# Kernel tuning notes

Hardware: AMD Instinct MI355X
Metric: run time of the kernel (lower is better)

The kernel has to match this reference:

```python
import jax, jax.numpy as jnp
import numpy as np

N = 50000       # nodes
E = 800000      # edges (before self-loops)
F_IN = 128      # num_features
HID = 32        # hidden_dim per head
HEADS = 8
C = 40          # num_classes
NEG_SLOPE = 0.2 # PyG GATConv default leaky_relu slope


def setup_inputs() -> dict:
    key = jax.random.key(0)
    ks = jax.random.split(key, 10)
    x = jax.random.normal(ks[0], (N, F_IN), jnp.float32)
    edge_index = jax.random.randint(ks[1], (2, E), 0, N, dtype=jnp.int64)
    W1 = jax.random.normal(ks[2], (F_IN, HEADS * HID), jnp.float32) * np.float32(1.0 / np.sqrt(F_IN))
    a1_src = jax.random.normal(ks[3], (HEADS, HID), jnp.float32) * 0.1
    a1_dst = jax.random.normal(ks[4], (HEADS, HID), jnp.float32) * 0.1
    b1 = jnp.zeros((HEADS * HID,), jnp.float32)
    W2 = jax.random.normal(ks[5], (HEADS * HID, C), jnp.float32) * np.float32(1.0 / np.sqrt(HEADS * HID))
    a2_src = jax.random.normal(ks[6], (1, C), jnp.float32) * 0.1
    a2_dst = jax.random.normal(ks[7], (1, C), jnp.float32) * 0.1
    b2 = jnp.zeros((C,), jnp.float32)
    return {"x": x, "edge_index": edge_index,
            "W1": W1, "a1_src": a1_src, "a1_dst": a1_dst, "b1": b1,
            "W2": W2, "a2_src": a2_src, "a2_dst": a2_dst, "b2": b2}


def gat_conv(x, edge_index, W, a_src, a_dst, bias):
    """PyG-style GATConv (concat heads, add_self_loops=True), inference mode (no dropout)."""
    n = x.shape[0]
    heads, out_dim = a_src.shape
    ar = jnp.arange(n, dtype=edge_index.dtype)
    src = jnp.concatenate([edge_index[0], ar])   # [E+N]
    dst = jnp.concatenate([edge_index[1], ar])   # [E+N]
    h = (x @ W).reshape(n, heads, out_dim)       # [N, H, D]
    alpha_src = jnp.einsum('nhd,hd->nh', h, a_src)  # [N, H]
    alpha_dst = jnp.einsum('nhd,hd->nh', h, a_dst)  # [N, H]
    e = jax.nn.leaky_relu(alpha_src[src] + alpha_dst[dst], NEG_SLOPE)  # [E+N, H]
    # segment softmax over edges grouped by destination node
    m = jax.ops.segment_max(e, dst, num_segments=n)          # [N, H]
    ex = jnp.exp(e - m[dst])                                  # [E+N, H]
    s = jax.ops.segment_sum(ex, dst, num_segments=n)          # [N, H]
    alpha = ex / (s[dst] + 1e-16)                              # [E+N, H]
    msg = h[src] * alpha[..., None]                            # [E+N, H, D]
    out = jax.ops.segment_sum(msg, dst, num_segments=n)       # [N, H, D]
    return out.reshape(n, heads * out_dim) + bias


def reference(x, edge_index, W1, a1_src, a1_dst, b1, W2, a2_src, a2_dst, b2):
    h = jax.nn.elu(gat_conv(x, edge_index, W1, a1_src, a1_dst, b1))
    # F.dropout is identity in eval mode
    return gat_conv(h, edge_index, W2, a2_src, a2_dst, b2)
```

## Files before the change

### kernel.cpp

```cpp
#include <hip/hip_runtime.h>
#include <math.h>

#define F_IN 128
#define HID 32
#define HEADS 8
#define HD 256
#define NC 40
#define NCP 48
#define H2S 64
#define CAP 96
#define NEG 0.2f

typedef _Float16 half8 __attribute__((ext_vector_type(8)));
typedef float f32x4 __attribute__((ext_vector_type(4)));

__device__ __forceinline__ float leaky(float v) { return v > 0.0f ? v : NEG * v; }
__device__ __forceinline__ float2 up2(unsigned int u) {
    union { unsigned int u; _Float16 h[2]; } c; c.u = u;
    return make_float2((float)c.h[0], (float)c.h[1]);
}

__global__ __launch_bounds__(256) void prep_scatter_k(const int* __restrict__ ei,
        int* __restrict__ cnt, int* __restrict__ esrc,
        const float* __restrict__ W1, const float* __restrict__ W2,
        const float* __restrict__ a1s, const float* __restrict__ a1d,
        _Float16* __restrict__ W1t, _Float16* __restrict__ W2t,
        _Float16* __restrict__ Pt, int E) {
    int i = blockIdx.x * 256 + threadIdx.x;
    if (i < E) {
        int src = ei[i], dst = ei[E + i];
        int pos = atomicAdd(&cnt[dst], 1);
        esrc[dst * CAP + pos] = src;
        return;
    }
    int w1i = i - E;
    if (w1i < HD * F_IN) {
        int c = w1i >> 7, k = w1i & 127;
        W1t[w1i] = (_Float16)W1[k * HD + c];
        return;
    }
    int w2i = w1i - HD * F_IN;
    if (w2i < NCP * HD) {
        int c = w2i >> 8, k = w2i & 255;
        W2t[w2i] = (c < NC) ? (_Float16)W2[k * NC + c] : (_Float16)0.0f;
        return;
    }
    int p = w2i - NCP * HD;
    if (p < 16 * F_IN) {
        int pj = p >> 7, k = p & 127;
        int h = pj & 7;
        const float* av = (pj < 8) ? (a1s + h * HID) : (a1d + h * HID);
        const float* wr = W1 + (size_t)k * HD + h * HID;
        float acc = 0.0f;
#pragma unroll 8
        for (int d = 0; d < HID; ++d) acc = fmaf(wr[d], av[d], acc);
        Pt[pj * F_IN + k] = (_Float16)acc;
    }
}

__global__ __launch_bounds__(256) void gemm1_k(const float* __restrict__ x,
        const _Float16* __restrict__ W1t, const _Float16* __restrict__ Pt,
        _Float16* __restrict__ H1, float* __restrict__ asrc,
        float* __restrict__ adst, int N) {
    int t = threadIdx.x;
    int w = t >> 6, l = t & 63;
    int quad = l >> 4, lr = l & 15;
    int rowA = blockIdx.x * 64 + w * 16 + lr;
    int rowL = rowA < N ? rowA : N - 1;

    half8 af[4];
    const float* xr = x + (size_t)rowL * F_IN + quad * 8;
#pragma unroll
    for (int s = 0; s < 4; ++s) {
        float4 u = *(const float4*)(xr + s * 32);
        float4 v = *(const float4*)(xr + s * 32 + 4);
        half8 a;
        a[0] = (_Float16)u.x; a[1] = (_Float16)u.y;
        a[2] = (_Float16)u.z; a[3] = (_Float16)u.w;
        a[4] = (_Float16)v.x; a[5] = (_Float16)v.y;
        a[6] = (_Float16)v.z; a[7] = (_Float16)v.w;
        af[s] = a;
    }

    int rowC0 = blockIdx.x * 64 + w * 16 + quad * 4;
#pragma unroll
    for (int tt = 0; tt < 16; ++tt) {
        f32x4 acc = {0.0f, 0.0f, 0.0f, 0.0f};
        const _Float16* wp = W1t + (size_t)(tt * 16 + lr) * F_IN + quad * 8;
#pragma unroll
        for (int s = 0; s < 4; ++s) {
            half8 b = *(const half8*)(wp + s * 32);
            acc = __builtin_amdgcn_mfma_f32_16x16x32_f16(af[s], b, acc, 0, 0, 0);
        }
#pragma unroll
        for (int r = 0; r < 4; ++r) {
            int rr = rowC0 + r;
            if (rr < N) H1[(size_t)rr * HD + tt * 16 + lr] = (_Float16)acc[r];
        }
    }
    {
        f32x4 acc = {0.0f, 0.0f, 0.0f, 0.0f};
        const _Float16* pp = Pt + (size_t)lr * F_IN + quad * 8;
#pragma unroll
        for (int s = 0; s < 4; ++s) {
            half8 b = *(const half8*)(pp + s * 32);
            acc = __builtin_amdgcn_mfma_f32_16x16x32_f16(af[s], b, acc, 0, 0, 0);
        }
#pragma unroll
        for (int r = 0; r < 4; ++r) {
            int rr = rowC0 + r;
            if (rr < N) {
                if (lr < 8) asrc[rr * HEADS + lr] = acc[r];
                else        adst[rr * HEADS + (lr - 8)] = acc[r];
            }
        }
    }
}

__global__ __launch_bounds__(256) void agg1_k(const int* __restrict__ esrc,
        const int* __restrict__ cnt, const float* __restrict__ asrc,
        const float* __restrict__ adst, const _Float16* __restrict__ H1,
        const float* __restrict__ b1, _Float16* __restrict__ out1, int N) {
    int t = threadIdx.x;
    int c = t & 31;
    int dst = blockIdx.x * 8 + (t >> 5);
    if (dst >= N) return;
    int h = c >> 2;
    int start = dst * CAP;
    int end = start + cnt[dst];
    float adh = adst[dst * HEADS + h];

    float ws = __expf(leaky(asrc[dst * HEADS + h] + adh));
    float s = ws;
    float acc[8];
    {
        uint4 hs = *(const uint4*)(H1 + (size_t)dst * HD + c * 8);
        float2 p0 = up2(hs.x), p1 = up2(hs.y), p2 = up2(hs.z), p3 = up2(hs.w);
        acc[0] = p0.x * ws; acc[1] = p0.y * ws;
        acc[2] = p1.x * ws; acc[3] = p1.y * ws;
        acc[4] = p2.x * ws; acc[5] = p2.y * ws;
        acc[6] = p3.x * ws; acc[7] = p3.y * ws;
    }

    int e = start;
    for (; e + 3 < end; e += 4) {
        int si[4]; float al[4]; uint4 hv[4];
#pragma unroll
        for (int q = 0; q < 4; ++q) si[q] = esrc[e + q];
#pragma unroll
        for (int q = 0; q < 4; ++q) {
            al[q] = asrc[si[q] * HEADS + h];
            hv[q] = *(const uint4*)(H1 + (size_t)si[q] * HD + c * 8);
        }
#pragma unroll
        for (int q = 0; q < 4; ++q) {
            float w = __expf(leaky(al[q] + adh));
            s += w;
            float2 p0 = up2(hv[q].x), p1 = up2(hv[q].y);
            float2 p2 = up2(hv[q].z), p3 = up2(hv[q].w);
            acc[0] = fmaf(p0.x, w, acc[0]); acc[1] = fmaf(p0.y, w, acc[1]);
            acc[2] = fmaf(p1.x, w, acc[2]); acc[3] = fmaf(p1.y, w, acc[3]);
            acc[4] = fmaf(p2.x, w, acc[4]); acc[5] = fmaf(p2.y, w, acc[5]);
            acc[6] = fmaf(p3.x, w, acc[6]); acc[7] = fmaf(p3.y, w, acc[7]);
        }
    }
    for (; e < end; ++e) {
        int s0 = esrc[e];
        float al0 = asrc[s0 * HEADS + h];
        uint4 h0 = *(const uint4*)(H1 + (size_t)s0 * HD + c * 8);
        float w0 = __expf(leaky(al0 + adh));
        s += w0;
        float2 p0 = up2(h0.x), p1 = up2(h0.y);
        float2 p2 = up2(h0.z), p3 = up2(h0.w);
        acc[0] = fmaf(p0.x, w0, acc[0]); acc[1] = fmaf(p0.y, w0, acc[1]);
        acc[2] = fmaf(p1.x, w0, acc[2]); acc[3] = fmaf(p1.y, w0, acc[3]);
        acc[4] = fmaf(p2.x, w0, acc[4]); acc[5] = fmaf(p2.y, w0, acc[5]);
        acc[6] = fmaf(p3.x, w0, acc[6]); acc[7] = fmaf(p3.y, w0, acc[7]);
    }
    float inv = 1.0f / (s + 1e-16f);
    float4 b0 = *(const float4*)(b1 + c * 8);
    float4 b4 = *(const float4*)(b1 + c * 8 + 4);
    float o[8];
    o[0] = fmaf(acc[0], inv, b0.x); o[1] = fmaf(acc[1], inv, b0.y);
    o[2] = fmaf(acc[2], inv, b0.z); o[3] = fmaf(acc[3], inv, b0.w);
    o[4] = fmaf(acc[4], inv, b4.x); o[5] = fmaf(acc[5], inv, b4.y);
    o[6] = fmaf(acc[6], inv, b4.z); o[7] = fmaf(acc[7], inv, b4.w);
    half8 ov;
#pragma unroll
    for (int q = 0; q < 8; ++q) {
        float v = o[q] > 0.0f ? o[q] : expm1f(o[q]);
        ov[q] = (_Float16)v;
    }
    *(half8*)(out1 + (size_t)dst * HD + c * 8) = ov;
}

__global__ __launch_bounds__(256) void gemm2_k(const _Float16* __restrict__ out1,
        const _Float16* __restrict__ W2t, const float* __restrict__ a2s,
        const float* __restrict__ a2d, _Float16* __restrict__ H2h,
        float* __restrict__ asrc2, float* __restrict__ adst2, int N) {
    int t = threadIdx.x;
    int w = t >> 6, l = t & 63;
    int quad = l >> 4, lr = l & 15;
    int rowA = blockIdx.x * 64 + w * 16 + lr;
    int rowL = rowA < N ? rowA : N - 1;

    half8 af[8];
    const _Float16* ar = out1 + (size_t)rowL * HD + quad * 8;
#pragma unroll
    for (int s = 0; s < 8; ++s) af[s] = *(const half8*)(ar + s * 32);

    f32x4 acc[3];
#pragma unroll
    for (int tt = 0; tt < 3; ++tt) {
        f32x4 a = {0.0f, 0.0f, 0.0f, 0.0f};
        const _Float16* wp = W2t + (size_t)(tt * 16 + lr) * HD + quad * 8;
#pragma unroll
        for (int s = 0; s < 8; ++s) {
            half8 b = *(const half8*)(wp + s * 32);
            a = __builtin_amdgcn_mfma_f32_16x16x32_f16(af[s], b, a, 0, 0, 0);
        }
        acc[tt] = a;
    }

    float a2sv[3], a2dv[3];
#pragma unroll
    for (int tt = 0; tt < 3; ++tt) {
        int col = tt * 16 + lr;
        a2sv[tt] = (col < NC) ? a2s[col] : 0.0f;
        a2dv[tt] = (col < NC) ? a2d[col] : 0.0f;
    }
    int rowC0 = blockIdx.x * 64 + w * 16 + quad * 4;
#pragma unroll
    for (int r = 0; r < 4; ++r) {
        int row = rowC0 + r;
        if (row >= N) break;
        float ps = 0.0f, pd = 0.0f;
#pragma unroll
        for (int tt = 0; tt < 3; ++tt) {
            int col = tt * 16 + lr;
            float v = acc[tt][r];
            H2h[(size_t)row * H2S + col] = (_Float16)v;
            ps = fmaf(v, a2sv[tt], ps);
            pd = fmaf(v, a2dv[tt], pd);
        }
        ps += __shfl_xor(ps, 1, 64); ps += __shfl_xor(ps, 2, 64);
        ps += __shfl_xor(ps, 4, 64); ps += __shfl_xor(ps, 8, 64);
        pd += __shfl_xor(pd, 1, 64); pd += __shfl_xor(pd, 2, 64);
        pd += __shfl_xor(pd, 4, 64); pd += __shfl_xor(pd, 8, 64);
        if (lr == 0) { asrc2[row] = ps; adst2[row] = pd; }
    }
}

__global__ __launch_bounds__(256) void agg2_k(const int* __restrict__ esrc,
        const int* __restrict__ cnt, const float* __restrict__ asrc,
        const float* __restrict__ adst, const _Float16* __restrict__ H2h,
        const float* __restrict__ b2, float* __restrict__ dout, int N) {
    int t = threadIdx.x;
    int c = t & 31;
    int dst = blockIdx.x * 8 + (t >> 5);
    if (dst >= N) return;
    int start = dst * CAP;
    int end = start + cnt[dst];
    float adst_v = adst[dst];

    float ws = __expf(leaky(asrc[dst] + adst_v));
    float s = ws;
    float a0, a1;
    {
        unsigned int hv = *(const unsigned int*)(H2h + (size_t)dst * H2S + c * 2);
        float2 p = up2(hv);
        a0 = p.x * ws; a1 = p.y * ws;
    }

    int e = start;
    for (; e + 7 < end; e += 8) {
        int si[8]; float al[8]; unsigned int v[8];
#pragma unroll
        for (int q = 0; q < 8; ++q) si[q] = esrc[e + q];
#pragma unroll
        for (int q = 0; q < 8; ++q) {
            al[q] = asrc[si[q]];
            v[q] = *(const unsigned int*)(H2h + (size_t)si[q] * H2S + c * 2);
        }
#pragma unroll
        for (int q = 0; q < 8; ++q) {
            float w = __expf(leaky(al[q] + adst_v));
            s += w;
            float2 p = up2(v[q]);
            a0 = fmaf(p.x, w, a0);
            a1 = fmaf(p.y, w, a1);
        }
    }
    for (; e + 3 < end; e += 4) {
        int si[4]; float al[4]; unsigned int v[4];
#pragma unroll
        for (int q = 0; q < 4; ++q) si[q] = esrc[e + q];
#pragma unroll
        for (int q = 0; q < 4; ++q) {
            al[q] = asrc[si[q]];
            v[q] = *(const unsigned int*)(H2h + (size_t)si[q] * H2S + c * 2);
        }
#pragma unroll
        for (int q = 0; q < 4; ++q) {
            float w = __expf(leaky(al[q] + adst_v));
            s += w;
            float2 p = up2(v[q]);
            a0 = fmaf(p.x, w, a0);
            a1 = fmaf(p.y, w, a1);
        }
    }
    for (; e < end; ++e) {
        int s0 = esrc[e];
        float w0 = __expf(leaky(asrc[s0] + adst_v));
        s += w0;
        float2 p = up2(*(const unsigned int*)(H2h + (size_t)s0 * H2S + c * 2));
        a0 = fmaf(p.x, w0, a0);
        a1 = fmaf(p.y, w0, a1);
    }
    if (c * 2 < NC) {
        float inv = 1.0f / (s + 1e-16f);
        float2 o;
        o.x = fmaf(a0, inv, b2[c * 2]);
        o.y = fmaf(a1, inv, b2[c * 2 + 1]);
        *(float2*)(dout + (size_t)dst * NC + c * 2) = o;
    }
}

extern "C" void kernel_launch(void* const* d_in, const int* in_sizes, int n_in,
                              void* d_out, int out_size, void* d_ws, size_t ws_size,
                              hipStream_t stream) {
    const float* x   = (const float*)d_in[0];
    const int*   ei  = (const int*)d_in[1];
    const float* W1  = (const float*)d_in[2];
    const float* a1s = (const float*)d_in[3];
    const float* a1d = (const float*)d_in[4];
    const float* b1  = (const float*)d_in[5];
    const float* W2  = (const float*)d_in[6];
    const float* a2s = (const float*)d_in[7];
    const float* a2d = (const float*)d_in[8];
    const float* b2  = (const float*)d_in[9];
    float* dout = (float*)d_out;

    int N = in_sizes[0] / F_IN;
    int E = in_sizes[1] / 2;

    char* base = (char*)d_ws;
    size_t off = 0;
    auto carve = [&](size_t bytes) { char* p = base + off; off += (bytes + 255) & ~(size_t)255; return p; };
    _Float16* H1   = (_Float16*)carve((size_t)N * HD * 2);
    _Float16* W1t  = (_Float16*)carve((size_t)HD * F_IN * 2);
    _Float16* W2t  = (_Float16*)carve((size_t)NCP * HD * 2);
    _Float16* Pt   = (_Float16*)carve((size_t)16 * F_IN * 2);
    _Float16* out1 = (_Float16*)carve((size_t)N * HD * 2);
    _Float16* H2h  = (_Float16*)carve((size_t)N * H2S * 2);
    float* asrc1  = (float*)carve((size_t)N * HEADS * 4);
    float* adst1  = (float*)carve((size_t)N * HEADS * 4);
    float* asrc2  = (float*)carve((size_t)N * 4);
    float* adst2  = (float*)carve((size_t)N * 4);
    int*   cnt    = (int*)carve((size_t)N * 4);
    int*   esrc   = (int*)carve((size_t)N * CAP * 4);

    hipMemsetAsync(cnt, 0, (size_t)N * 4, stream);
    int prep_total = E + HD * F_IN + NCP * HD + 16 * F_IN;
    hipLaunchKernelGGL(prep_scatter_k, dim3((prep_total + 255) / 256), dim3(256), 0, stream,
                       ei, cnt, esrc, W1, W2, a1s, a1d, W1t, W2t, Pt, E);

    hipLaunchKernelGGL(gemm1_k, dim3((N + 63) / 64), dim3(256), 0, stream,
                       x, W1t, Pt, H1, asrc1, adst1, N);
    hipLaunchKernelGGL(agg1_k, dim3((N + 7) / 8), dim3(256), 0, stream,
                       esrc, cnt, asrc1, adst1, H1, b1, out1, N);

    hipLaunchKernelGGL(gemm2_k, dim3((N + 63) / 64), dim3(256), 0, stream,
                       out1, W2t, a2s, a2d, H2h, asrc2, adst2, N);
    hipLaunchKernelGGL(agg2_k, dim3((N + 7) / 8), dim3(256), 0, stream,
                       esrc, cnt, asrc2, adst2, H2h, b2, dout, N);
}
```

Measured before the change: 282.2 us.

## Store layer-1 features head-major so aggregation gathers per-head slabs

```diff
diff --git a/kernel.cpp b/kernel.cpp
--- a/kernel.cpp
+++ b/kernel.cpp
@@ -60,8 +60,8 @@
 
 __global__ __launch_bounds__(256) void gemm1_k(const float* __restrict__ x,
         const _Float16* __restrict__ W1t, const _Float16* __restrict__ Pt,
-        _Float16* __restrict__ H1, float* __restrict__ asrc,
-        float* __restrict__ adst, int N) {
+        _Float16* __restrict__ H1s, float* __restrict__ asrcT,
+        float* __restrict__ adstT, int N) {
     int t = threadIdx.x;
     int w = t >> 6, l = t & 63;
     int quad = l >> 4, lr = l & 15;
@@ -95,7 +95,8 @@
 #pragma unroll
         for (int r = 0; r < 4; ++r) {
             int rr = rowC0 + r;
-            if (rr < N) H1[(size_t)rr * HD + tt * 16 + lr] = (_Float16)acc[r];
+            if (rr < N)
+                H1s[((size_t)(tt >> 1) * N + rr) * 32 + (tt & 1) * 16 + lr] = (_Float16)acc[r];
         }
     }
     {
@@ -110,31 +111,33 @@
         for (int r = 0; r < 4; ++r) {
             int rr = rowC0 + r;
             if (rr < N) {
-                if (lr < 8) asrc[rr * HEADS + lr] = acc[r];
-                else        adst[rr * HEADS + (lr - 8)] = acc[r];
+                if (lr < 8) asrcT[(size_t)lr * N + rr] = acc[r];
+                else        adstT[(size_t)(lr - 8) * N + rr] = acc[r];
             }
         }
     }
 }
 
 __global__ __launch_bounds__(256) void agg1_k(const int* __restrict__ esrc,
-        const int* __restrict__ cnt, const float* __restrict__ asrc,
-        const float* __restrict__ adst, const _Float16* __restrict__ H1,
+        const int* __restrict__ cnt, const float* __restrict__ asrcT,
+        const float* __restrict__ adstT, const _Float16* __restrict__ H1s,
         const float* __restrict__ b1, _Float16* __restrict__ out1, int N) {
     int t = threadIdx.x;
-    int c = t & 31;
-    int dst = blockIdx.x * 8 + (t >> 5);
+    int p = blockIdx.x & 7;
+    int dst = (blockIdx.x >> 3) * 64 + (t >> 2);
     if (dst >= N) return;
-    int h = c >> 2;
+    int j = t & 3;
+    const _Float16* Hp = H1s + (size_t)p * N * 32;
+    const float* ap = asrcT + (size_t)p * N;
+    float adh = adstT[(size_t)p * N + dst];
     int start = dst * CAP;
     int end = start + cnt[dst];
-    float adh = adst[dst * HEADS + h];
-
-    float ws = __expf(leaky(asrc[dst * HEADS + h] + adh));
+
+    float ws = __expf(leaky(ap[dst] + adh));
     float s = ws;
     float acc[8];
     {
-        uint4 hs = *(const uint4*)(H1 + (size_t)dst * HD + c * 8);
+        uint4 hs = *(const uint4*)(Hp + (size_t)dst * 32 + j * 8);
         float2 p0 = up2(hs.x), p1 = up2(hs.y), p2 = up2(hs.z), p3 = up2(hs.w);
         acc[0] = p0.x * ws; acc[1] = p0.y * ws;
         acc[2] = p1.x * ws; acc[3] = p1.y * ws;
@@ -149,8 +152,8 @@
         for (int q = 0; q < 4; ++q) si[q] = esrc[e + q];
 #pragma unroll
         for (int q = 0; q < 4; ++q) {
-            al[q] = asrc[si[q] * HEADS + h];
-            hv[q] = *(const uint4*)(H1 + (size_t)si[q] * HD + c * 8);
+            al[q] = ap[si[q]];
+            hv[q] = *(const uint4*)(Hp + (size_t)si[q] * 32 + j * 8);
         }
 #pragma unroll
         for (int q = 0; q < 4; ++q) {
@@ -166,8 +169,8 @@
     }
     for (; e < end; ++e) {
         int s0 = esrc[e];
-        float al0 = asrc[s0 * HEADS + h];
-        uint4 h0 = *(const uint4*)(H1 + (size_t)s0 * HD + c * 8);
+        float al0 = ap[s0];
+        uint4 h0 = *(const uint4*)(Hp + (size_t)s0 * 32 + j * 8);
         float w0 = __expf(leaky(al0 + adh));
         s += w0;
         float2 p0 = up2(h0.x), p1 = up2(h0.y);
@@ -178,8 +181,9 @@
         acc[6] = fmaf(p3.x, w0, acc[6]); acc[7] = fmaf(p3.y, w0, acc[7]);
     }
     float inv = 1.0f / (s + 1e-16f);
-    float4 b0 = *(const float4*)(b1 + c * 8);
-    float4 b4 = *(const float4*)(b1 + c * 8 + 4);
+    const float* bp = b1 + p * 32 + j * 8;
+    float4 b0 = *(const float4*)(bp);
+    float4 b4 = *(const float4*)(bp + 4);
     float o[8];
     o[0] = fmaf(acc[0], inv, b0.x); o[1] = fmaf(acc[1], inv, b0.y);
     o[2] = fmaf(acc[2], inv, b0.z); o[3] = fmaf(acc[3], inv, b0.w);
@@ -191,7 +195,7 @@
         float v = o[q] > 0.0f ? o[q] : expm1f(o[q]);
         ov[q] = (_Float16)v;
     }
-    *(half8*)(out1 + (size_t)dst * HD + c * 8) = ov;
+    *(half8*)(out1 + (size_t)dst * HD + p * 32 + j * 8) = ov;
 }
 
 __global__ __launch_bounds__(256) void gemm2_k(const _Float16* __restrict__ out1,
@@ -347,14 +351,14 @@
     char* base = (char*)d_ws;
     size_t off = 0;
     auto carve = [&](size_t bytes) { char* p = base + off; off += (bytes + 255) & ~(size_t)255; return p; };
-    _Float16* H1   = (_Float16*)carve((size_t)N * HD * 2);
+    _Float16* H1s  = (_Float16*)carve((size_t)N * HD * 2);
     _Float16* W1t  = (_Float16*)carve((size_t)HD * F_IN * 2);
     _Float16* W2t  = (_Float16*)carve((size_t)NCP * HD * 2);
     _Float16* Pt   = (_Float16*)carve((size_t)16 * F_IN * 2);
     _Float16* out1 = (_Float16*)carve((size_t)N * HD * 2);
     _Float16* H2h  = (_Float16*)carve((size_t)N * H2S * 2);
-    float* asrc1  = (float*)carve((size_t)N * HEADS * 4);
-    float* adst1  = (float*)carve((size_t)N * HEADS * 4);
+    float* asrcT  = (float*)carve((size_t)N * HEADS * 4);
+    float* adstT  = (float*)carve((size_t)N * HEADS * 4);
     float* asrc2  = (float*)carve((size_t)N * 4);
     float* adst2  = (float*)carve((size_t)N * 4);
     int*   cnt    = (int*)carve((size_t)N * 4);
@@ -366,9 +370,9 @@
                        ei, cnt, esrc, W1, W2, a1s, a1d, W1t, W2t, Pt, E);
 
     hipLaunchKernelGGL(gemm1_k, dim3((N + 63) / 64), dim3(256), 0, stream,
-                       x, W1t, Pt, H1, asrc1, adst1, N);
-    hipLaunchKernelGGL(agg1_k, dim3((N + 7) / 8), dim3(256), 0, stream,
-                       esrc, cnt, asrc1, adst1, H1, b1, out1, N);
+                       x, W1t, Pt, H1s, asrcT, adstT, N);
+    hipLaunchKernelGGL(agg1_k, dim3(((N + 63) / 64) * 8), dim3(256), 0, stream,
+                       esrc, cnt, asrcT, adstT, H1s, b1, out1, N);
 
     hipLaunchKernelGGL(gemm2_k, dim3((N + 63) / 64), dim3(256), 0, stream,
                        out1, W2t, a2s, a2d, H2h, asrc2, adst2, N);
```

After: 293.6 us. 4.1% more time.

## Fuse layer-2 GEMM into layer-1 aggregation and fold attention vectors into W2

Applied to the files above, without the earlier changes.

```diff
diff --git a/kernel.cpp b/kernel.cpp
--- a/kernel.cpp
+++ b/kernel.cpp
@@ -24,6 +24,7 @@
         int* __restrict__ cnt, int* __restrict__ esrc,
         const float* __restrict__ W1, const float* __restrict__ W2,
         const float* __restrict__ a1s, const float* __restrict__ a1d,
+        const float* __restrict__ a2s, const float* __restrict__ a2d,
         _Float16* __restrict__ W1t, _Float16* __restrict__ W2t,
         _Float16* __restrict__ Pt, int E) {
     int i = blockIdx.x * 256 + threadIdx.x;
@@ -42,7 +43,14 @@
     int w2i = w1i - HD * F_IN;
     if (w2i < NCP * HD) {
         int c = w2i >> 8, k = w2i & 255;
-        W2t[w2i] = (c < NC) ? (_Float16)W2[k * NC + c] : (_Float16)0.0f;
+        float v = 0.0f;
+        if (c < NC) {
+            v = W2[k * NC + c];
+        } else if (c == NC || c == NC + 1) {
+            const float* av = (c == NC) ? a2s : a2d;
+            for (int d = 0; d < NC; ++d) v = fmaf(W2[k * NC + d], av[d], v);
+        }
+        W2t[w2i] = (_Float16)v;
         return;
     }
     int p = w2i - NCP * HD;
@@ -117,24 +125,28 @@
     }
 }
 
-__global__ __launch_bounds__(256) void agg1_k(const int* __restrict__ esrc,
+__global__ __launch_bounds__(256) void agg1g2_k(const int* __restrict__ esrc,
         const int* __restrict__ cnt, const float* __restrict__ asrc,
         const float* __restrict__ adst, const _Float16* __restrict__ H1,
-        const float* __restrict__ b1, _Float16* __restrict__ out1, int N) {
+        const float* __restrict__ b1, const _Float16* __restrict__ W2t,
+        _Float16* __restrict__ H2h, float* __restrict__ asrc2,
+        float* __restrict__ adst2, int N) {
+    __shared__ _Float16 rows[16][HD];
     int t = threadIdx.x;
     int c = t & 31;
-    int dst = blockIdx.x * 8 + (t >> 5);
-    if (dst >= N) return;
+    int ld = t >> 5;
+    int dst = blockIdx.x * 8 + ld;
+    int dstc = dst < N ? dst : N - 1;
     int h = c >> 2;
-    int start = dst * CAP;
-    int end = start + cnt[dst];
-    float adh = adst[dst * HEADS + h];
-
-    float ws = __expf(leaky(asrc[dst * HEADS + h] + adh));
+    int start = dstc * CAP;
+    int end = start + cnt[dstc];
+    float adh = adst[dstc * HEADS + h];
+
+    float ws = __expf(leaky(asrc[dstc * HEADS + h] + adh));
     float s = ws;
     float acc[8];
     {
-        uint4 hs = *(const uint4*)(H1 + (size_t)dst * HD + c * 8);
+        uint4 hs = *(const uint4*)(H1 + (size_t)dstc * HD + c * 8);
         float2 p0 = up2(hs.x), p1 = up2(hs.y), p2 = up2(hs.z), p3 = up2(hs.w);
         acc[0] = p0.x * ws; acc[1] = p0.y * ws;
         acc[2] = p1.x * ws; acc[3] = p1.y * ws;
@@ -185,69 +197,53 @@
     o[2] = fmaf(acc[2], inv, b0.z); o[3] = fmaf(acc[3], inv, b0.w);
     o[4] = fmaf(acc[4], inv, b4.x); o[5] = fmaf(acc[5], inv, b4.y);
     o[6] = fmaf(acc[6], inv, b4.z); o[7] = fmaf(acc[7], inv, b4.w);
-    half8 ov;
+    half8 ov, zv;
 #pragma unroll
     for (int q = 0; q < 8; ++q) {
         float v = o[q] > 0.0f ? o[q] : expm1f(o[q]);
         ov[q] = (_Float16)v;
-    }
-    *(half8*)(out1 + (size_t)dst * HD + c * 8) = ov;
-}
-
-__global__ __launch_bounds__(256) void gemm2_k(const _Float16* __restrict__ out1,
-        const _Float16* __restrict__ W2t, const float* __restrict__ a2s,
-        const float* __restrict__ a2d, _Float16* __restrict__ H2h,
-        float* __restrict__ asrc2, float* __restrict__ adst2, int N) {
-    int t = threadIdx.x;
-    int w = t >> 6, l = t & 63;
-    int quad = l >> 4, lr = l & 15;
-    int rowA = blockIdx.x * 64 + w * 16 + lr;
-    int rowL = rowA < N ? rowA : N - 1;
-
-    half8 af[8];
-    const _Float16* ar = out1 + (size_t)rowL * HD + quad * 8;
-#pragma unroll
-    for (int s = 0; s < 8; ++s) af[s] = *(const half8*)(ar + s * 32);
-
-    f32x4 acc[3];
-#pragma unroll
-    for (int tt = 0; tt < 3; ++tt) {
-        f32x4 a = {0.0f, 0.0f, 0.0f, 0.0f};
-        const _Float16* wp = W2t + (size_t)(tt * 16 + lr) * HD + quad * 8;
-#pragma unroll
-        for (int s = 0; s < 8; ++s) {
-            half8 b = *(const half8*)(wp + s * 32);
-            a = __builtin_amdgcn_mfma_f32_16x16x32_f16(af[s], b, a, 0, 0, 0);
-        }
-        acc[tt] = a;
-    }
-
-    float a2sv[3], a2dv[3];
-#pragma unroll
-    for (int tt = 0; tt < 3; ++tt) {
-        int col = tt * 16 + lr;
-        a2sv[tt] = (col < NC) ? a2s[col] : 0.0f;
-        a2dv[tt] = (col < NC) ? a2d[col] : 0.0f;
-    }
-    int rowC0 = blockIdx.x * 64 + w * 16 + quad * 4;
-#pragma unroll
-    for (int r = 0; r < 4; ++r) {
-        int row = rowC0 + r;
-        if (row >= N) break;
-        float ps = 0.0f, pd = 0.0f;
+        zv[q] = (_Float16)0.0f;
+    }
+    *(half8*)&rows[ld][c * 8] = ov;
+    *(half8*)&rows[8 + ld][c * 8] = zv;
+    __syncthreads();
+
+    if (t < 64) {
+        int quad = t >> 4, lr = t & 15;
+        half8 af[8];
+#pragma unroll
+        for (int sfs = 0; sfs < 8; ++sfs)
+            af[sfs] = *(const half8*)&rows[lr][sfs * 32 + quad * 8];
+        f32x4 ga[3];
 #pragma unroll
         for (int tt = 0; tt < 3; ++tt) {
-            int col = tt * 16 + lr;
-            float v = acc[tt][r];
-            H2h[(size_t)row * H2S + col] = (_Float16)v;
-            ps = fmaf(v, a2sv[tt], ps);
-            pd = fmaf(v, a2dv[tt], pd);
-        }
-        ps += __shfl_xor(ps, 1, 64); ps += __shfl_xor(ps, 2, 64);
-        ps += __shfl_xor(ps, 4, 64); ps += __shfl_xor(ps, 8, 64);
-        pd += __shfl_xor(pd, 1, 64); pd += __shfl_xor(pd, 2, 64);
-        pd += __shfl_xor(pd, 4, 64); pd += __shfl_xor(pd, 8, 64);
-        if (lr == 0) { asrc2[row] = ps; adst2[row] = pd; }
+            f32x4 a = {0.0f, 0.0f, 0.0f, 0.0f};
+            const _Float16* wp = W2t + (size_t)(tt * 16 + lr) * HD + quad * 8;
+#pragma unroll
+            for (int sfs = 0; sfs < 8; ++sfs) {
+                half8 b = *(const half8*)(wp + sfs * 32);
+                a = __builtin_amdgcn_mfma_f32_16x16x32_f16(af[sfs], b, a, 0, 0, 0);
+            }
+            ga[tt] = a;
+        }
+        int row0 = quad * 4;
+#pragma unroll
+        for (int tt = 0; tt < 3; ++tt) {
+            int c2 = tt * 16 + lr;
+#pragma unroll
+            for (int r = 0; r < 4; ++r) {
+                int row = row0 + r;
+                if (row < 8) {
+                    int g = blockIdx.x * 8 + row;
+                    if (g < N) {
+                        float v = ga[tt][r];
+                        if (c2 < NC)            H2h[(size_t)g * H2S + c2] = (_Float16)v;
+                        else if (c2 == NC)      asrc2[g] = v;
+                        else if (c2 == NC + 1)  adst2[g] = v;
+                    }
+                }
+            }
+        }
     }
 }
 
@@ -351,7 +347,6 @@
     _Float16* W1t  = (_Float16*)carve((size_t)HD * F_IN * 2);
     _Float16* W2t  = (_Float16*)carve((size_t)NCP * HD * 2);
     _Float16* Pt   = (_Float16*)carve((size_t)16 * F_IN * 2);
-    _Float16* out1 = (_Float16*)carve((size_t)N * HD * 2);
     _Float16* H2h  = (_Float16*)carve((size_t)N * H2S * 2);
     float* asrc1  = (float*)carve((size_t)N * HEADS * 4);
     float* adst1  = (float*)carve((size_t)N * HEADS * 4);
@@ -363,15 +358,12 @@
     hipMemsetAsync(cnt, 0, (size_t)N * 4, stream);
     int prep_total = E + HD * F_IN + NCP * HD + 16 * F_IN;
     hipLaunchKernelGGL(prep_scatter_k, dim3((prep_total + 255) / 256), dim3(256), 0, stream,
-                       ei, cnt, esrc, W1, W2, a1s, a1d, W1t, W2t, Pt, E);
+                       ei, cnt, esrc, W1, W2, a1s, a1d, a2s, a2d, W1t, W2t, Pt, E);
 
     hipLaunchKernelGGL(gemm1_k, dim3((N + 63) / 64), dim3(256), 0, stream,
                        x, W1t, Pt, H1, asrc1, adst1, N);
-    hipLaunchKernelGGL(agg1_k, dim3((N + 7) / 8), dim3(256), 0, stream,
-                       esrc, cnt, asrc1, adst1, H1, b1, out1, N);
-
-    hipLaunchKernelGGL(gemm2_k, dim3((N + 63) / 64), dim3(256), 0, stream,
-                       out1, W2t, a2s, a2d, H2h, asrc2, adst2, N);
+    hipLaunchKernelGGL(agg1g2_k, dim3((N + 7) / 8), dim3(256), 0, stream,
+                       esrc, cnt, asrc1, adst1, H1, b1, W2t, H2h, asrc2, adst2, N);
     hipLaunchKernelGGL(agg2_k, dim3((N + 7) / 8), dim3(256), 0, stream,
                        esrc, cnt, asrc2, adst2, H2h, b2, dout, N);
 }
```

New measurement: 268.8 us. -4.7%, faster.
